# Kernel optimization log

Measured on AMD Instinct MI355X. Metric: run time of the kernel, lower is better.

## Reference

```python
import jax, jax.numpy as jnp
import numpy as np

LYR, H, NH, B, L = 2, 512, 32, 8, 4096


def setup_inputs() -> dict:
    key = jax.random.key(0)
    ks = jax.random.split(key, 24)
    rn = lambda i, shape, s=1.0: s * jax.random.normal(ks[i], shape, dtype=jnp.float32)
    w_scale = 1.0 / np.sqrt(H)
    # S4D-Lin style init: A = -0.5 + i*pi*n, dt log-uniform in [1e-3, 1e-1]
    A_im = (np.pi * jnp.arange(NH, dtype=jnp.float32))[None, None, :] * jnp.ones((LYR, H, NH), jnp.float32)
    log_dt = jnp.log(1e-3) + jax.random.uniform(ks[1], (LYR, H), dtype=jnp.float32) * (jnp.log(1e-1) - jnp.log(1e-3))
    return {
        "x": rn(0, (B, L, H)),
        "ln1_w": jnp.ones((LYR, H), jnp.float32),
        "ln1_b": jnp.zeros((LYR, H), jnp.float32),
        "ln2_w": jnp.ones((LYR, H), jnp.float32),
        "ln2_b": jnp.zeros((LYR, H), jnp.float32),
        "log_dt": log_dt,
        "A_re": -0.5 * jnp.ones((LYR, H, NH), jnp.float32),
        "A_im": A_im,
        "B_re": jnp.ones((LYR, H, NH), jnp.float32) + rn(2, (LYR, H, NH), 0.1),
        "B_im": rn(3, (LYR, H, NH), 0.1),
        "C_re": rn(4, (LYR, H, NH), 0.5),
        "C_im": rn(5, (LYR, H, NH), 0.5),
        "D": rn(6, (LYR, H)),
        "Wk": rn(7, (LYR, H, H), w_scale),
        "bk": jnp.zeros((LYR, H), jnp.float32),
        "W1": rn(8, (LYR, H, H), w_scale),
        "b1": jnp.zeros((LYR, H), jnp.float32),
        "W2": rn(9, (LYR, H, H), w_scale),
        "b2": jnp.zeros((LYR, H), jnp.float32),
        "Wout": rn(10, (LYR, H, H), w_scale),
        "bout": jnp.zeros((LYR, H), jnp.float32),
        "Wproj": rn(11, (LYR, H, H), w_scale),
        "bproj": jnp.zeros((LYR, H), jnp.float32),
    }


def _layer_norm(x, g, b, eps=1e-5):
    m = jnp.mean(x, axis=-1, keepdims=True)
    v = jnp.mean((x - m) ** 2, axis=-1, keepdims=True)
    return (x - m) * jax.lax.rsqrt(v + eps) * g + b


def _ssm_kernel(log_dt, A_re, A_im, B_re, B_im, C_re, C_im, Lseq):
    # ZOH-discretized diagonal SSM kernel (conjugate-symmetric -> 2*real)
    dt = jnp.exp(log_dt)[:, None]                    # [H,1]
    A = A_re + 1j * A_im                             # [H,NH]
    dtA = dt * A
    dA = jnp.exp(dtA)
    dB = (B_re + 1j * B_im) * (dA - 1.0) / A
    coef = (C_re + 1j * C_im) * dB                   # [H,NH]
    t = jnp.arange(Lseq, dtype=jnp.float32)
    V = jnp.exp(dtA[:, :, None] * t)                 # Vandermonde [H,NH,L]
    return 2.0 * jnp.einsum('hn,hnl->hl', coef, V).real  # [H,L]


def _fft_conv(u, K):
    # causal long convolution via FFT; u: [B,L,H], K: [H,L]
    n = 2 * u.shape[1]
    Uf = jnp.fft.rfft(u, n=n, axis=1)                # [B,n/2+1,H]
    Kf = jnp.fft.rfft(K, n=n, axis=-1)               # [H,n/2+1]
    y = jnp.fft.irfft(Uf * Kf.T[None], n=n, axis=1)[:, :u.shape[1]]
    return y


def reference(x, ln1_w, ln1_b, ln2_w, ln2_b, log_dt, A_re, A_im, B_re, B_im,
              C_re, C_im, D, Wk, bk, W1, b1, W2, b2, Wout, bout, Wproj, bproj):
    out = x
    n_layers = ln1_w.shape[0]
    for l in range(n_layers):
        z = _layer_norm(out, ln1_w[l], ln1_b[l])
        # S4 layer: kernel gen + FFT conv + D skip + gelu + output linear
        K = _ssm_kernel(log_dt[l], A_re[l], A_im[l], B_re[l], B_im[l],
                        C_re[l], C_im[l], z.shape[1])
        y = _fft_conv(z, K) + z * D[l]
        y = jax.nn.gelu(y, approximate=False)
        y = y @ Wk[l] + bk[l]
        # residual branch 1
        o1 = y @ W1[l] + b1[l] + out
        # FFN-like branch with projection residual
        z2 = _layer_norm(o1, ln2_w[l], ln2_b[l])
        h = jax.nn.gelu(z2 @ W2[l] + b2[l], approximate=False)
        out = h @ Wout[l] + bout[l] + (o1 @ Wproj[l] + bproj[l])
    return out
```

## Files before the change

### kernel.cpp

```cpp
#include <hip/hip_runtime.h>
#include <hip/hip_bf16.h>
#include <math.h>

#define LYR   2
#define H     512
#define NH    32
#define BATCH 8
#define SEQL  4096
#define QC    64
#define NC    (SEQL / QC)
#define MROWS (BATCH * SEQL)

typedef __attribute__((ext_vector_type(8))) short short8;
typedef __attribute__((ext_vector_type(4))) float floatx4;
typedef __hip_bfloat16 bf16;

__device__ __forceinline__ float gelu_f(float x) {
    return 0.5f * x * (1.0f + erff(x * 0.70710678118654752440f));
}

__device__ __forceinline__ void glds16(const void* g, void* l) {
    __builtin_amdgcn_global_load_lds((const __attribute__((address_space(1))) void*)g,
                                     (__attribute__((address_space(3))) void*)l, 16, 0, 0);
}

__global__ void cast_w_kernel(const float* __restrict__ W, bf16* __restrict__ Wt) {
    __shared__ __align__(16) float tile[64][65];
    const int l  = blockIdx.z;
    const int k0 = blockIdx.y * 64;
    const int n0 = blockIdx.x * 64;
    const float* src = W + (size_t)l * H * H;
    bf16* dst = Wt + (size_t)l * H * H;
#pragma unroll
    for (int i = 0; i < 16; i++) {
        int e = i * 256 + threadIdx.x;
        int r = e >> 6, c = e & 63;
        tile[r][c] = src[(size_t)(k0 + r) * H + n0 + c];
    }
    __syncthreads();
#pragma unroll
    for (int i = 0; i < 16; i++) {
        int e = i * 256 + threadIdx.x;
        int r = e >> 6, c = e & 63;
        dst[(size_t)(n0 + r) * H + k0 + c] = __float2bfloat16(tile[c][r]);
    }
}

__global__ void ssm_params_kernel(const float* __restrict__ log_dt,
                                  const float* __restrict__ A_re, const float* __restrict__ A_im,
                                  const float* __restrict__ B_re, const float* __restrict__ B_im,
                                  const float* __restrict__ C_re, const float* __restrict__ C_im,
                                  float* __restrict__ dA, float* __restrict__ coef,
                                  float* __restrict__ dAQ) {
    const int idx = blockIdx.x * 256 + threadIdx.x;
    if (idx >= LYR * H * NH) return;
    const int lh = idx >> 5;
    const float dt  = expf(log_dt[lh]);
    const float are = A_re[idx], aim = A_im[idx];
    const float e   = expf(dt * are);
    const float dre = e * cosf(dt * aim);
    const float dim_ = e * sinf(dt * aim);
    const float den = are * are + aim * aim;
    const float nre = dre - 1.0f, nim = dim_;
    const float qre = (nre * are + nim * aim) / den;
    const float qim = (nim * are - nre * aim) / den;
    const float bre = B_re[idx], bim = B_im[idx];
    const float dbre = bre * qre - bim * qim;
    const float dbim = bre * qim + bim * qre;
    const float cre = C_re[idx], cim = C_im[idx];
    coef[2 * idx]     = cre * dbre - cim * dbim;
    coef[2 * idx + 1] = cre * dbim + cim * dbre;
    dA[2 * idx]     = dre;
    dA[2 * idx + 1] = dim_;
    const float eq = expf((float)QC * dt * are);
    const float ph = (float)QC * dt * aim;
    dAQ[2 * idx]     = eq * cosf(ph);
    dAQ[2 * idx + 1] = eq * sinf(ph);
}

__global__ void prep_mats(const float* __restrict__ dA, const float* __restrict__ coef,
                          const float* __restrict__ Dv,
                          bf16* __restrict__ M1b, bf16* __restrict__ TEb) {
    const int lh = blockIdx.x;
    const int t  = threadIdx.x;
    __shared__ float Ksh[64];
    const float* dAp = dA + (size_t)lh * NH * 2;
    const float* cfp = coef + (size_t)lh * NH * 2;
    bf16* terow = TEb + ((size_t)lh * 64 + t) * 192;
    float Kt = 0.f;
    for (int n = 0; n < NH; n++) {
        const float dre = dAp[2 * n], dim_ = dAp[2 * n + 1];
        const float cre = cfp[2 * n], cim = cfp[2 * n + 1];
        float pr = 1.f, pi = 0.f;
        for (int i = 0; i < t; i++) { float tr = pr * dre - pi * dim_; pi = pr * dim_ + pi * dre; pr = tr; }
        Kt += 2.f * (cre * pr - cim * pi);
        const float per = pr * dre - pi * dim_;
        const float pei = pr * dim_ + pi * dre;
        const float e0 = 2.f * (cre * per - cim * pei);
        const float e1 = -2.f * (cre * pei + cim * per);
        terow[64 + 2 * n]      = __float2bfloat16(e0);
        terow[64 + 2 * n + 1]  = __float2bfloat16(e1);
        terow[128 + 2 * n]     = __float2bfloat16(e0);
        terow[128 + 2 * n + 1] = __float2bfloat16(e1);
        float qr = 1.f, qi = 0.f;
        for (int i = 0; i < 63 - t; i++) { float tr = qr * dre - qi * dim_; qi = qr * dim_ + qi * dre; qr = tr; }
        M1b[((size_t)lh * 64 + 2 * n) * 64 + t]     = __float2bfloat16(qr);
        M1b[((size_t)lh * 64 + 2 * n + 1) * 64 + t] = __float2bfloat16(qi);
    }
    Ksh[t] = Kt;
    __syncthreads();
    const float Dh = Dv[lh];
    for (int tau = 0; tau < 64; tau++) {
        float v = (tau > t) ? 0.f : Ksh[t - tau];
        if (tau == t) v += Dh;
        terow[tau] = __float2bfloat16(v);
    }
}

__global__ void ln_kernel(const float* __restrict__ src,
                          const float* __restrict__ gamma, const float* __restrict__ beta,
                          bf16* __restrict__ outb) {
    const int lane = threadIdx.x & 63;
    const int row  = blockIdx.x * 4 + (threadIdx.x >> 6);
    const float4* rp = (const float4*)(src + (size_t)row * H);
    float4 v0 = rp[lane];
    float4 v1 = rp[64 + lane];
    float s = v0.x + v0.y + v0.z + v0.w + v1.x + v1.y + v1.z + v1.w;
    float q = v0.x * v0.x + v0.y * v0.y + v0.z * v0.z + v0.w * v0.w +
              v1.x * v1.x + v1.y * v1.y + v1.z * v1.z + v1.w * v1.w;
#pragma unroll
    for (int off = 32; off > 0; off >>= 1) {
        s += __shfl_xor(s, off);
        q += __shfl_xor(q, off);
    }
    const float mean = s * (1.0f / H);
    const float var  = q * (1.0f / H) - mean * mean;
    const float rstd = rsqrtf(var + 1e-5f);
    const float4* gp = (const float4*)gamma;
    const float4* bp = (const float4*)beta;
    float4 g0 = gp[lane], g1 = gp[64 + lane];
    float4 b0 = bp[lane], b1 = bp[64 + lane];
    bf16 t0[4] = {__float2bfloat16((v0.x - mean) * rstd * g0.x + b0.x),
                  __float2bfloat16((v0.y - mean) * rstd * g0.y + b0.y),
                  __float2bfloat16((v0.z - mean) * rstd * g0.z + b0.z),
                  __float2bfloat16((v0.w - mean) * rstd * g0.w + b0.w)};
    bf16 t1[4] = {__float2bfloat16((v1.x - mean) * rstd * g1.x + b1.x),
                  __float2bfloat16((v1.y - mean) * rstd * g1.y + b1.y),
                  __float2bfloat16((v1.z - mean) * rstd * g1.z + b1.z),
                  __float2bfloat16((v1.w - mean) * rstd * g1.w + b1.w)};
    *(uint2*)(outb + (size_t)row * H + lane * 4)       = *(uint2*)t0;
    *(uint2*)(outb + (size_t)row * H + 256 + lane * 4) = *(uint2*)t1;
}

__global__ void trans_in_k(const bf16* __restrict__ z, bf16* __restrict__ Ub) {
    const int hb = blockIdx.x & 7, bc = blockIdx.x >> 3;
    const int b = bc >> 6, c = bc & 63;
    const int h0 = hb * 64;
    __shared__ __align__(16) ushort Ti[64][68];
    const ushort* zp = (const ushort*)z + ((size_t)b * SEQL + c * QC) * H + h0;
#pragma unroll
    for (int i = 0; i < 4; i++) {
        int tau = i * 16 + (threadIdx.x >> 4), h4 = (threadIdx.x & 15) * 4;
        *(ushort4*)&Ti[tau][h4] = *(const ushort4*)(zp + (size_t)tau * H + h4);
    }
    __syncthreads();
    ushort* up = (ushort*)Ub + ((size_t)h0 * 512 + bc) * 64;
#pragma unroll
    for (int i = 0; i < 4; i++) {
        int hh = i * 16 + (threadIdx.x >> 4), t4 = (threadIdx.x & 15) * 4;
        ushort4 v;
        v.x = Ti[t4][hh]; v.y = Ti[t4 + 1][hh]; v.z = Ti[t4 + 2][hh]; v.w = Ti[t4 + 3][hh];
        *(ushort4*)(up + (size_t)hh * 512 * 64 + t4) = v;
    }
}

__global__ void conv_p1(const bf16* __restrict__ M1l, const bf16* __restrict__ Ub,
                        float* __restrict__ Sloc) {
    const int h = blockIdx.x >> 2;
    const int n0 = (blockIdx.x & 3) * 128;
    __shared__ __align__(16) bf16 As[64][72];
    __shared__ __align__(16) bf16 Bs[128][72];
    const int tid = threadIdx.x, lane = tid & 63, wid = tid >> 6;
    const int wm = (wid & 1) * 32, wn = (wid >> 1) * 64;
#pragma unroll
    for (int i = 0; i < 2; i++) {
        int idx = i * 256 + tid, r = idx >> 3, c8 = (idx & 7) * 8;
        *(floatx4*)&As[r][c8] = *(const floatx4*)(M1l + ((size_t)h * 64 + r) * 64 + c8);
    }
#pragma unroll
    for (int i = 0; i < 4; i++) {
        int idx = i * 256 + tid, r = idx >> 3, c8 = (idx & 7) * 8;
        *(floatx4*)&Bs[r][c8] = *(const floatx4*)(Ub + ((size_t)h * 512 + n0 + r) * 64 + c8);
    }
    __syncthreads();
    floatx4 acc[2][4] = {};
#pragma unroll
    for (int ks = 0; ks < 64; ks += 32) {
        short8 af[2], bfr[4];
#pragma unroll
        for (int mt = 0; mt < 2; mt++)
            af[mt] = *(const short8*)&As[wm + mt * 16 + (lane & 15)][ks + (lane >> 4) * 8];
#pragma unroll
        for (int nt = 0; nt < 4; nt++)
            bfr[nt] = *(const short8*)&Bs[wn + nt * 16 + (lane & 15)][ks + (lane >> 4) * 8];
#pragma unroll
        for (int mt = 0; mt < 2; mt++)
#pragma unroll
            for (int nt = 0; nt < 4; nt++)
                acc[mt][nt] = __builtin_amdgcn_mfma_f32_16x16x32_bf16(af[mt], bfr[nt], acc[mt][nt], 0, 0, 0);
    }
#pragma unroll
    for (int mt = 0; mt < 2; mt++)
#pragma unroll
        for (int nt = 0; nt < 4; nt++) {
            const int bc = n0 + wn + nt * 16 + (lane & 15);
#pragma unroll
            for (int r = 0; r < 4; r++) {
                const int j = wm + mt * 16 + ((lane >> 4) << 2) + r;
                Sloc[((size_t)h * 64 + j) * 512 + bc] = acc[mt][nt][r];
            }
        }
}

__global__ void conv_scan2(const float* __restrict__ Sloc, const float* __restrict__ dAQl,
                           bf16* __restrict__ S0b) {
    const int h = blockIdx.x >> 3, b = blockIdx.x & 7;
    const int tid = threadIdx.x;
    __shared__ __align__(16) float Sl[64][65];
    __shared__ __align__(16) bf16 Ob[64][128];
#pragma unroll
    for (int i = 0; i < 16; i++) {
        int j = i * 4 + (tid >> 6), c = tid & 63;
        Sl[j][c] = Sloc[((size_t)h * 64 + j) * 512 + b * 64 + c];
    }
    __syncthreads();
    if (tid < 32) {
        const int n = tid;
        const float qr = dAQl[(h * NH + n) * 2], qi = dAQl[(h * NH + n) * 2 + 1];
        float rr = 0.f, ri = 0.f;
        for (int c = 0; c < 64; c++) {
            bf16 hr = __float2bfloat16(rr);
            bf16 hi = __float2bfloat16(ri);
            Ob[c][2 * n]          = hr;
            Ob[c][2 * n + 1]      = hi;
            Ob[c][64 + 2 * n]     = __float2bfloat16(rr - __bfloat162float(hr));
            Ob[c][64 + 2 * n + 1] = __float2bfloat16(ri - __bfloat162float(hi));
            const float lr = Sl[2 * n][c], li = Sl[2 * n + 1][c];
            const float tr = qr * rr - qi * ri + lr;
            ri = qr * ri + qi * rr + li;
            rr = tr;
        }
    }
    __syncthreads();
    bf16* op = S0b + ((size_t)h * 512 + b * 64) * 128;
#pragma unroll
    for (int i = 0; i < 4; i++) {
        int idx = i * 256 + tid, c = idx >> 4, c8 = (idx & 15) * 8;
        *(floatx4*)(op + (size_t)c * 128 + c8) = *(const floatx4*)&Ob[c][c8];
    }
}

__global__ void conv_p3(const bf16* __restrict__ TEl, const bf16* __restrict__ Ub,
                        const bf16* __restrict__ S0b, bf16* __restrict__ Yt) {
    const int h = blockIdx.x >> 2;
    const int n0 = (blockIdx.x & 3) * 128;
    __shared__ __align__(16) char sm3[(64 + 128) * 200 * 2];
    bf16(*As)[200] = (bf16(*)[200])sm3;
    bf16(*Bs)[200] = (bf16(*)[200])(sm3 + 64 * 200 * 2);
    const int tid = threadIdx.x, lane = tid & 63, wid = tid >> 6;
    const int wm = (wid & 1) * 32, wn = (wid >> 1) * 64;
#pragma unroll
    for (int i = 0; i < 6; i++) {
        int idx = i * 256 + tid, r = idx / 24, c = (idx - r * 24) * 8;
        *(floatx4*)&As[r][c] = *(const floatx4*)(TEl + ((size_t)h * 64 + r) * 192 + c);
    }
#pragma unroll
    for (int i = 0; i < 4; i++) {
        int idx = i * 256 + tid, r = idx >> 3, c8 = (idx & 7) * 8;
        *(floatx4*)&Bs[r][c8] = *(const floatx4*)(Ub + ((size_t)h * 512 + n0 + r) * 64 + c8);
    }
#pragma unroll
    for (int i = 0; i < 8; i++) {
        int idx = i * 256 + tid, r = idx >> 4, c8 = (idx & 15) * 8;
        *(floatx4*)&Bs[r][64 + c8] = *(const floatx4*)(S0b + ((size_t)h * 512 + n0 + r) * 128 + c8);
    }
    __syncthreads();
    floatx4 acc[2][4] = {};
#pragma unroll
    for (int ks = 0; ks < 192; ks += 32) {
        short8 af[2], bfr[4];
#pragma unroll
        for (int mt = 0; mt < 2; mt++)
            af[mt] = *(const short8*)&As[wm + mt * 16 + (lane & 15)][ks + (lane >> 4) * 8];
#pragma unroll
        for (int nt = 0; nt < 4; nt++)
            bfr[nt] = *(const short8*)&Bs[wn + nt * 16 + (lane & 15)][ks + (lane >> 4) * 8];
#pragma unroll
        for (int mt = 0; mt < 2; mt++)
#pragma unroll
            for (int nt = 0; nt < 4; nt++)
                acc[mt][nt] = __builtin_amdgcn_mfma_f32_16x16x32_bf16(af[mt], bfr[nt], acc[mt][nt], 0, 0, 0);
    }
    __syncthreads();
    bf16(*Tt)[72] = (bf16(*)[72])sm3;
#pragma unroll
    for (int mt = 0; mt < 2; mt++)
#pragma unroll
        for (int nt = 0; nt < 4; nt++) {
            const int n = wn + nt * 16 + (lane & 15);
#pragma unroll
            for (int r = 0; r < 4; r++) {
                const int t = wm + mt * 16 + ((lane >> 4) << 2) + r;
                Tt[n][t] = __float2bfloat16(gelu_f(acc[mt][nt][r]));
            }
        }
    __syncthreads();
#pragma unroll
    for (int i = 0; i < 4; i++) {
        int idx = i * 256 + tid, r = idx >> 3, c8 = (idx & 7) * 8;
        *(floatx4*)(Yt + ((size_t)h * 512 + n0 + r) * 64 + c8) = *(const floatx4*)&Tt[r][c8];
    }
}

__global__ void trans_out_k(const bf16* __restrict__ Yt, bf16* __restrict__ y) {
    const int hb = blockIdx.x & 7, bc = blockIdx.x >> 3;
    const int b = bc >> 6, c = bc & 63;
    const int h0 = hb * 64;
    __shared__ __align__(16) ushort Ti[64][68];
    const ushort* yp = (const ushort*)Yt + ((size_t)h0 * 512 + bc) * 64;
#pragma unroll
    for (int i = 0; i < 4; i++) {
        int hh = i * 16 + (threadIdx.x >> 4), t4 = (threadIdx.x & 15) * 4;
        *(ushort4*)&Ti[hh][t4] = *(const ushort4*)(yp + (size_t)hh * 512 * 64 + t4);
    }
    __syncthreads();
    ushort* op = (ushort*)y + ((size_t)b * SEQL + c * QC) * H + h0;
#pragma unroll
    for (int i = 0; i < 4; i++) {
        int tau = i * 16 + (threadIdx.x >> 4), h4 = (threadIdx.x & 15) * 4;
        ushort4 v;
        v.x = Ti[h4][tau]; v.y = Ti[h4 + 1][tau]; v.z = Ti[h4 + 2][tau]; v.w = Ti[h4 + 3][tau];
        *(ushort4*)(op + (size_t)tau * H + h4) = v;
    }
}

enum { M_BIAS = 0, M_RES = 1, M_GELU = 2, M_DUAL = 3 };

template <int MODE>
__global__ void gemm_kernel(const bf16* __restrict__ A1, const bf16* __restrict__ Wt1,
                            const bf16* __restrict__ A2, const bf16* __restrict__ Wt2,
                            const float* __restrict__ bias1, const float* __restrict__ bias2,
                            const float* __restrict__ res,
                            float* __restrict__ outf, bf16* __restrict__ outb, int KTOT) {
    __shared__ __align__(16) bf16 As[128][64];
    __shared__ __align__(16) bf16 Bs[128][64];
    const int tid  = threadIdx.x;
    const int lane = tid & 63;
    const int wid  = tid >> 6;
    const int wm   = (wid >> 1) * 64;
    const int wn   = (wid & 1) * 64;
    const int m0   = blockIdx.y * 128;
    const int n0   = blockIdx.x * 128;

    floatx4 acc[4][4] = {};

    for (int k0 = 0; k0 < KTOT; k0 += 64) {
        const bf16* Ap;
        const bf16* Wp;
        int kk = k0;
        if (MODE == M_DUAL && k0 >= 512) { Ap = A2; Wp = Wt2; kk = k0 - 512; }
        else                             { Ap = A1; Wp = Wt1; }
#pragma unroll
        for (int i = 0; i < 4; i++) {
            const int s   = wid * 256 + i * 64 + lane;
            const int r   = s >> 3;
            const int cbg = (s & 7) ^ (r & 7);
            glds16(Ap + (size_t)(m0 + r) * 512 + kk + cbg * 8,
                   (char*)&As[0][0] + (size_t)(wid * 256 + i * 64) * 16);
            glds16(Wp + (size_t)(n0 + r) * 512 + kk + cbg * 8,
                   (char*)&Bs[0][0] + (size_t)(wid * 256 + i * 64) * 16);
        }
        __syncthreads();
#pragma unroll
        for (int ks = 0; ks < 64; ks += 32) {
            short8 af[4], bfr[4];
#pragma unroll
            for (int mt = 0; mt < 4; mt++) {
                const int row = wm + mt * 16 + (lane & 15);
                const int cph = ((ks >> 3) + (lane >> 4)) ^ (row & 7);
                af[mt] = *(const short8*)&As[row][cph * 8];
            }
#pragma unroll
            for (int nt = 0; nt < 4; nt++) {
                const int row = wn + nt * 16 + (lane & 15);
                const int cph = ((ks >> 3) + (lane >> 4)) ^ (row & 7);
                bfr[nt] = *(const short8*)&Bs[row][cph * 8];
            }
#pragma unroll
            for (int mt = 0; mt < 4; mt++)
#pragma unroll
                for (int nt = 0; nt < 4; nt++)
                    acc[mt][nt] = __builtin_amdgcn_mfma_f32_16x16x32_bf16(
                        af[mt], bfr[nt], acc[mt][nt], 0, 0, 0);
        }
        __syncthreads();
    }

#pragma unroll
    for (int mt = 0; mt < 4; mt++) {
        const int rbase = m0 + wm + mt * 16 + ((lane >> 4) << 2);
#pragma unroll
        for (int nt = 0; nt < 4; nt++) {
            const int col = n0 + wn + nt * 16 + (lane & 15);
            float bsum = bias1[col];
            if constexpr (MODE == M_DUAL) bsum += bias2[col];
#pragma unroll
            for (int r = 0; r < 4; r++) {
                const int row = rbase + r;
                float v = acc[mt][nt][r] + bsum;
                if constexpr (MODE == M_RES) v += res[(size_t)row * H + col];
                if constexpr (MODE == M_GELU) v = gelu_f(v);
                const size_t o = (size_t)row * H + col;
                if constexpr (MODE == M_RES || MODE == M_DUAL) outf[o] = v;
                if constexpr (MODE != M_DUAL) outb[o] = __float2bfloat16(v);
            }
        }
    }
}

extern "C" void kernel_launch(void* const* d_in, const int* in_sizes, int n_in,
                              void* d_out, int out_size, void* d_ws, size_t ws_size,
                              hipStream_t stream) {
    const float* x     = (const float*)d_in[0];
    const float* ln1w  = (const float*)d_in[1];
    const float* ln1b  = (const float*)d_in[2];
    const float* ln2w  = (const float*)d_in[3];
    const float* ln2b  = (const float*)d_in[4];
    const float* logdt = (const float*)d_in[5];
    const float* Are   = (const float*)d_in[6];
    const float* Aim   = (const float*)d_in[7];
    const float* Bre   = (const float*)d_in[8];
    const float* Bim   = (const float*)d_in[9];
    const float* Cre   = (const float*)d_in[10];
    const float* Cim   = (const float*)d_in[11];
    const float* Dvec  = (const float*)d_in[12];
    const float* Wk    = (const float*)d_in[13];
    const float* bk    = (const float*)d_in[14];
    const float* W1    = (const float*)d_in[15];
    const float* b1    = (const float*)d_in[16];
    const float* W2    = (const float*)d_in[17];
    const float* b2    = (const float*)d_in[18];
    const float* Wout  = (const float*)d_in[19];
    const float* bout  = (const float*)d_in[20];
    const float* Wproj = (const float*)d_in[21];
    const float* bproj = (const float*)d_in[22];
    float* outp = (float*)d_out;

    char* p = (char*)d_ws;
    auto carve = [&](size_t bytes) -> char* {
        char* r = p;
        p += (bytes + 255) & ~(size_t)255;
        return r;
    };
    bf16*  zbA  = (bf16*)carve((size_t)MROWS * H * 2);
    bf16*  Ub   = (bf16*)carve((size_t)H * 512 * 64 * 2);
    float* Sloc = (float*)carve((size_t)H * 64 * 512 * 4);
    bf16*  S0b  = (bf16*)carve((size_t)H * 512 * 128 * 2);
    bf16*  M1b  = (bf16*)carve((size_t)LYR * H * 64 * 64 * 2);
    bf16*  TEb  = (bf16*)carve((size_t)LYR * H * 64 * 192 * 2);
    float* dAb  = (float*)carve((size_t)LYR * H * NH * 2 * 4);
    float* cfb  = (float*)carve((size_t)LYR * H * NH * 2 * 4);
    float* dAQb = (float*)carve((size_t)LYR * H * NH * 2 * 4);
    bf16* wts[5];
    for (int i = 0; i < 5; i++) wts[i] = (bf16*)carve((size_t)LYR * H * H * 2);

    bf16*  Yt   = zbA;
    bf16*  bb1  = Ub;
    float* zbuf = Sloc;
    bf16*  bb0  = S0b;
    bf16*  bb2  = S0b + (size_t)MROWS * H;

    const float* wsrc[5] = {Wk, W1, W2, Wout, Wproj};
    {
        dim3 g(8, 8, LYR);
        for (int i = 0; i < 5; i++)
            cast_w_kernel<<<g, 256, 0, stream>>>(wsrc[i], wts[i]);
    }
    ssm_params_kernel<<<(LYR * H * NH) / 256, 256, 0, stream>>>(
        logdt, Are, Aim, Bre, Bim, Cre, Cim, dAb, cfb, dAQb);
    prep_mats<<<LYR * H, 64, 0, stream>>>(dAb, cfb, Dvec, M1b, TEb);

    const float* cur = x;
    for (int l = 0; l < LYR; l++) {
        ln_kernel<<<MROWS / 4, 256, 0, stream>>>(cur, ln1w + l * H, ln1b + l * H, zbA);
        trans_in_k<<<BATCH * NC * 8, 256, 0, stream>>>(zbA, Ub);
        conv_p1<<<H * 4, 256, 0, stream>>>(M1b + (size_t)l * H * 64 * 64, Ub, Sloc);
        conv_scan2<<<H * BATCH, 256, 0, stream>>>(Sloc, dAQb + (size_t)l * H * NH * 2, S0b);
        conv_p3<<<H * 4, 256, 0, stream>>>(TEb + (size_t)l * H * 64 * 192, Ub, S0b, Yt);
        trans_out_k<<<BATCH * NC * 8, 256, 0, stream>>>(Yt, bb0);

        dim3 gg(H / 128, MROWS / 128);
        gemm_kernel<M_BIAS><<<gg, 256, 0, stream>>>(
            bb0, wts[0] + (size_t)l * H * H, nullptr, nullptr,
            bk + l * H, nullptr, nullptr, nullptr, bb1, 512);
        gemm_kernel<M_RES><<<gg, 256, 0, stream>>>(
            bb1, wts[1] + (size_t)l * H * H, nullptr, nullptr,
            b1 + l * H, nullptr, cur, zbuf, bb0, 512);
        ln_kernel<<<MROWS / 4, 256, 0, stream>>>(zbuf, ln2w + l * H, ln2b + l * H, bb1);
        gemm_kernel<M_GELU><<<gg, 256, 0, stream>>>(
            bb1, wts[2] + (size_t)l * H * H, nullptr, nullptr,
            b2 + l * H, nullptr, nullptr, nullptr, bb2, 512);
        gemm_kernel<M_DUAL><<<gg, 256, 0, stream>>>(
            bb2, wts[3] + (size_t)l * H * H, bb0, wts[4] + (size_t)l * H * H,
            bout + l * H, bproj + l * H, nullptr, outp, nullptr, 1024);
        cur = outp;
    }
}
```

Baseline: 953.6 us.

## Compute SSM powers in closed form and stage prep_mats outputs in LDS

prep_mats used to build powers of dA by serial complex multiplication, up to 63 steps per mode per thread, with only 64 threads per block. It now evaluates each power directly as exp(t*dtA), using cos/sin, and spreads the modes over 256 threads with a shuffle reduction for K. Outputs are staged in shared memory and written out with 16-byte coalesced stores instead of strided scalar bf16 stores. This is a one-off setup kernel, so the effect on total time is bounded, and closed-form exponentials give slightly different rounding than repeated multiplication.

```diff
diff --git a/kernel.cpp b/kernel.cpp
--- a/kernel.cpp
+++ b/kernel.cpp
@@ -50,7 +50,7 @@
                                   const float* __restrict__ A_re, const float* __restrict__ A_im,
                                   const float* __restrict__ B_re, const float* __restrict__ B_im,
                                   const float* __restrict__ C_re, const float* __restrict__ C_im,
-                                  float* __restrict__ dA, float* __restrict__ coef,
+                                  float* __restrict__ dtA, float* __restrict__ coef,
                                   float* __restrict__ dAQ) {
     const int idx = blockIdx.x * 256 + threadIdx.x;
     if (idx >= LYR * H * NH) return;
@@ -70,50 +70,80 @@
     const float cre = C_re[idx], cim = C_im[idx];
     coef[2 * idx]     = cre * dbre - cim * dbim;
     coef[2 * idx + 1] = cre * dbim + cim * dbre;
-    dA[2 * idx]     = dre;
-    dA[2 * idx + 1] = dim_;
+    dtA[2 * idx]     = dt * are;
+    dtA[2 * idx + 1] = dt * aim;
     const float eq = expf((float)QC * dt * are);
     const float ph = (float)QC * dt * aim;
     dAQ[2 * idx]     = eq * cosf(ph);
     dAQ[2 * idx + 1] = eq * sinf(ph);
 }
 
-__global__ void prep_mats(const float* __restrict__ dA, const float* __restrict__ coef,
+__global__ void prep_mats(const float* __restrict__ dtA, const float* __restrict__ coef,
                           const float* __restrict__ Dv,
                           bf16* __restrict__ M1b, bf16* __restrict__ TEb) {
-    const int lh = blockIdx.x;
-    const int t  = threadIdx.x;
+    const int lh  = blockIdx.x;
+    const int tid = threadIdx.x;
+    const int t   = tid >> 2;
+    const int ng  = tid & 3;
     __shared__ float Ksh[64];
-    const float* dAp = dA + (size_t)lh * NH * 2;
-    const float* cfp = coef + (size_t)lh * NH * 2;
-    bf16* terow = TEb + ((size_t)lh * 64 + t) * 192;
+    __shared__ __align__(16) bf16 TE[64][192];
+    __shared__ __align__(16) bf16 M1s[64][64];
+
+    const float ft = (float)t;
     float Kt = 0.f;
-    for (int n = 0; n < NH; n++) {
-        const float dre = dAp[2 * n], dim_ = dAp[2 * n + 1];
-        const float cre = cfp[2 * n], cim = cfp[2 * n + 1];
-        float pr = 1.f, pi = 0.f;
-        for (int i = 0; i < t; i++) { float tr = pr * dre - pi * dim_; pi = pr * dim_ + pi * dre; pr = tr; }
-        Kt += 2.f * (cre * pr - cim * pi);
+#pragma unroll
+    for (int k = 0; k < 8; k++) {
+        const int n = ng * 8 + k;
+        const float dtr = dtA[((size_t)lh * NH + n) * 2];
+        const float dti = dtA[((size_t)lh * NH + n) * 2 + 1];
+        const float cre = coef[((size_t)lh * NH + n) * 2];
+        const float cim = coef[((size_t)lh * NH + n) * 2 + 1];
+        const float er  = expf(dtr);
+        const float dre = er * cosf(dti), dim_ = er * sinf(dti);
+        const float et = expf(ft * dtr);
+        const float pr = et * cosf(ft * dti), pi = et * sinf(ft * dti);
+        Kt = fmaf(2.f * cre, pr, fmaf(-2.f * cim, pi, Kt));
         const float per = pr * dre - pi * dim_;
         const float pei = pr * dim_ + pi * dre;
         const float e0 = 2.f * (cre * per - cim * pei);
         const float e1 = -2.f * (cre * pei + cim * per);
-        terow[64 + 2 * n]      = __float2bfloat16(e0);
-        terow[64 + 2 * n + 1]  = __float2bfloat16(e1);
-        terow[128 + 2 * n]     = __float2bfloat16(e0);
-        terow[128 + 2 * n + 1] = __float2bfloat16(e1);
-        float qr = 1.f, qi = 0.f;
-        for (int i = 0; i < 63 - t; i++) { float tr = qr * dre - qi * dim_; qi = qr * dim_ + qi * dre; qr = tr; }
-        M1b[((size_t)lh * 64 + 2 * n) * 64 + t]     = __float2bfloat16(qr);
-        M1b[((size_t)lh * 64 + 2 * n + 1) * 64 + t] = __float2bfloat16(qi);
-    }
-    Ksh[t] = Kt;
+        const bf16 b0 = __float2bfloat16(e0), b1 = __float2bfloat16(e1);
+        TE[t][64 + 2 * n]  = b0;
+        TE[t][65 + 2 * n]  = b1;
+        TE[t][128 + 2 * n] = b0;
+        TE[t][129 + 2 * n] = b1;
+        const float fq = (float)(63 - t);
+        const float eq = expf(fq * dtr);
+        const float qr = eq * cosf(fq * dti), qi = eq * sinf(fq * dti);
+        M1s[2 * n][t]     = __float2bfloat16(qr);
+        M1s[2 * n + 1][t] = __float2bfloat16(qi);
+    }
+    Kt += __shfl_xor(Kt, 1);
+    Kt += __shfl_xor(Kt, 2);
+    if (ng == 0) Ksh[t] = Kt;
     __syncthreads();
     const float Dh = Dv[lh];
-    for (int tau = 0; tau < 64; tau++) {
+#pragma unroll
+    for (int i = 0; i < 16; i++) {
+        const int tau = ng * 16 + i;
         float v = (tau > t) ? 0.f : Ksh[t - tau];
         if (tau == t) v += Dh;
-        terow[tau] = __float2bfloat16(v);
+        TE[t][tau] = __float2bfloat16(v);
+    }
+    __syncthreads();
+    bf16* tep = TEb + (size_t)lh * 64 * 192;
+    const bf16* tes = &TE[0][0];
+#pragma unroll
+    for (int i = 0; i < 6; i++) {
+        const int idx = i * 256 + tid;
+        *(floatx4*)(tep + (size_t)idx * 8) = *(const floatx4*)(tes + (size_t)idx * 8);
+    }
+    bf16* m1p = M1b + (size_t)lh * 64 * 64;
+    const bf16* m1s = &M1s[0][0];
+#pragma unroll
+    for (int i = 0; i < 2; i++) {
+        const int idx = i * 256 + tid;
+        *(floatx4*)(m1p + (size_t)idx * 8) = *(const floatx4*)(m1s + (size_t)idx * 8);
     }
 }
 
@@ -468,7 +498,7 @@
     bf16*  S0b  = (bf16*)carve((size_t)H * 512 * 128 * 2);
     bf16*  M1b  = (bf16*)carve((size_t)LYR * H * 64 * 64 * 2);
     bf16*  TEb  = (bf16*)carve((size_t)LYR * H * 64 * 192 * 2);
-    float* dAb  = (float*)carve((size_t)LYR * H * NH * 2 * 4);
+    float* dtAb = (float*)carve((size_t)LYR * H * NH * 2 * 4);
     float* cfb  = (float*)carve((size_t)LYR * H * NH * 2 * 4);
     float* dAQb = (float*)carve((size_t)LYR * H * NH * 2 * 4);
     bf16* wts[5];
@@ -487,8 +517,8 @@
             cast_w_kernel<<<g, 256, 0, stream>>>(wsrc[i], wts[i]);
     }
     ssm_params_kernel<<<(LYR * H * NH) / 256, 256, 0, stream>>>(
-        logdt, Are, Aim, Bre, Bim, Cre, Cim, dAb, cfb, dAQb);
-    prep_mats<<<LYR * H, 64, 0, stream>>>(dAb, cfb, Dvec, M1b, TEb);
+        logdt, Are, Aim, Bre, Bim, Cre, Cim, dtAb, cfb, dAQb);
+    prep_mats<<<LYR * H, 256, 0, stream>>>(dtAb, cfb, Dvec, M1b, TEb);
 
     const float* cur = x;
     for (int l = 0; l < LYR; l++) {
```

After: 818.6 us. 14.2% less time.
